# Kernel tuning notes

Measured on AMD Instinct MI355X. Metric: run time of the kernel, lower is better.

## Reference

```python
import jax, jax.numpy as jnp
import numpy as np

# NOBlock config: no_dims_in=(8,8), input_dim=output_dim=128, rank=8, level_diff=1
B, N, V = 4, 2048, 1
G1, G2, C = 8, 8, 128   # in_shape = (8, 8, 128); m = G1*G2 = 64 grid cells per token
M = G1 * G2
R = 8                    # Tucker ranks: [8, 8, 8] in and out (min(dim, rank))
LEVEL_DIFF = 1
GRP = 4 ** LEVEL_DIFF    # quadtree group size for hierarchical residual


def _xavier(key, shape):
    lim = float(np.sqrt(6.0 / (shape[0] + shape[1])))
    return jax.random.uniform(key, shape, jnp.float32, -lim, lim)


def setup_inputs() -> dict:
    key = jax.random.key(0)
    ks = jax.random.split(key, 10)
    x = jax.random.normal(ks[0], (B, N, V, M, C), jnp.float32)
    # core ~ N(0, scale^2), scale = sqrt(2/(fan_in+fan_out)), fan = prod(ranks) = 8^3
    scale = float(np.sqrt(2.0 / (R ** 3 + R ** 3)))
    core = jax.random.normal(ks[1], (R, R, R, R, R, R), jnp.float32) * scale
    out_f0 = _xavier(ks[2], (G1, R))
    out_f1 = _xavier(ks[3], (G2, R))
    out_f2 = _xavier(ks[4], (C, R))
    in_f0 = _xavier(ks[5], (G1, R))
    in_f1 = _xavier(ks[6], (G2, R))
    in_f2 = _xavier(ks[7], (C, R))
    mask = jax.random.bernoulli(ks[8], 0.25, (B, N, M))  # True = masked cell
    return {"x": x, "core": core, "out_f0": out_f0, "out_f1": out_f1,
            "out_f2": out_f2, "in_f0": in_f0, "in_f1": in_f1, "in_f2": in_f2,
            "mask": mask}


def reference(x, core, out_f0, out_f1, out_f2, in_f0, in_f1, in_f2, mask):
    b, n, v = x.shape[:3]
    # --- CrossTuckerLayer: 'bnvade,ABCDEF,oA,pB,qC,aD,dE,eF->bnvopq' ---
    xr = x.reshape(b, n, v, G1, G2, C)
    # project onto in-factor rank spaces
    z = jnp.einsum('bnvade,aD,dE,eF->bnvDEF', xr, in_f0, in_f1, in_f2, optimize=True)
    # core contraction (out-ranks ABC x in-ranks DEF)
    z = jnp.einsum('bnvDEF,ABCDEF->bnvABC', z, core)
    # expand to output dims
    h = jnp.einsum('bnvABC,oA,pB,qC->bnvopq', z, out_f0, out_f1, out_f2, optimize=True)
    h = h.reshape(b, n, v, M, C)
    # residual connection
    h = h + x
    # --- get_residual: hierarchical masked mixing, level_diff = 1 ---
    h4 = h.reshape(b, n * v, M, C)                     # v = 1
    hg = h4.reshape(b, -1, GRP, M, C)                  # [b, n/4, 4, m, c]
    w = (~mask).reshape(b, -1, GRP, M, 1).sum(axis=2, keepdims=True).astype(h.dtype)
    out = (hg / (w + 1e-10)).sum(axis=2)               # [b, n/4, m, c]
    out = out * (w.sum(axis=2) != 0).astype(h.dtype)
    return out
```

## Files before the change

kernel.cpp:

```cpp
#include <hip/hip_runtime.h>
#include <cstdint>
#include <cstddef>


__device__ __forceinline__ float dot4(const float4 a, const float4 b, float s) {
    return fmaf(a.w, b.w, fmaf(a.z, b.z, fmaf(a.y, b.y, fmaf(a.x, b.x, s))));
}

__global__ void transpose_core(const float* __restrict__ core,
                               float* __restrict__ coreT) {
    const int tid = blockIdx.x * 256 + threadIdx.x;
    const int r = tid & 511, k4 = tid >> 9;
    ((float4*)coreT)[(size_t)k4 * 512 + r] =
        ((const float4*)core)[(size_t)r * 128 + k4];
}

__launch_bounds__(256, 3)
__global__ void k1_inproj(const float* __restrict__ x,
                          const float* __restrict__ if0,
                          const float* __restrict__ if1,
                          const float* __restrict__ if2,
                          float* __restrict__ xsum_out,
                          float* __restrict__ zz_ws)
{
    __shared__ float xs[64 * 132];
    __shared__ float t1[512];
    __shared__ float s_if2T[8 * 132];
    __shared__ float s_if0[64], s_if1[64];
    float* t2 = xs;

    const int t = threadIdx.x;
    const int g = blockIdx.x;

    for (int i = t; i < 1024; i += 256) {
        const int e = i & 127, F = i >> 7;
        s_if2T[F * 132 + e] = if2[e * 8 + F];
    }
    if (t < 64) { s_if0[t] = if0[t]; s_if1[t] = if1[t]; }

    const float4* xg4 = (const float4*)(x + (size_t)g * 4 * 8192);
    float4 acc[8];
    #pragma unroll
    for (int i = 0; i < 8; ++i) acc[i] = xg4[t + 256 * i];
    #pragma unroll
    for (int j = 1; j < 4; ++j) {
        float4 v[8];
        #pragma unroll
        for (int i = 0; i < 8; ++i) v[i] = xg4[(size_t)j * 2048 + t + 256 * i];
        #pragma unroll
        for (int i = 0; i < 8; ++i) {
            acc[i].x += v[i].x; acc[i].y += v[i].y;
            acc[i].z += v[i].z; acc[i].w += v[i].w;
        }
    }
    float4* xo = (float4*)xsum_out + (size_t)g * 2048;
    #pragma unroll
    for (int i = 0; i < 8; ++i) xo[t + 256 * i] = acc[i];
    #pragma unroll
    for (int i = 0; i < 8; ++i) {
        const int f4i = t + 256 * i;
        *(float4*)&xs[(f4i >> 5) * 132 + (f4i & 31) * 4] = acc[i];
    }
    __syncthreads();

    #pragma unroll
    for (int h = 0; h < 2; ++h) {
        const int id = t + 256 * h;
        const int m = id >> 3, F = id & 7;
        const float4* xr = (const float4*)(xs + m * 132);
        const float4* wr = (const float4*)(s_if2T + F * 132);
        float s0 = 0.f, s1 = 0.f;
        #pragma unroll
        for (int e4 = 0; e4 < 32; e4 += 2) {
            s0 = dot4(xr[e4],     wr[e4],     s0);
            s1 = dot4(xr[e4 + 1], wr[e4 + 1], s1);
        }
        t1[id] = s0 + s1;
    }
    __syncthreads();

    #pragma unroll
    for (int h = 0; h < 2; ++h) {
        const int id = t + 256 * h;
        const int E = id >> 6, a = (id >> 3) & 7, F = id & 7;
        float s = 0.f;
        #pragma unroll
        for (int d0 = 0; d0 < 8; ++d0) {
            const int d = (d0 + a) & 7;
            s = fmaf(t1[a * 64 + d * 8 + F], s_if1[d * 8 + E], s);
        }
        t2[id] = s;
    }
    __syncthreads();

    #pragma unroll
    for (int h = 0; h < 2; ++h) {
        const int id = t + 256 * h;
        const int D = id >> 6, E = (id >> 3) & 7, F = id & 7;
        float s = 0.f;
        #pragma unroll
        for (int a0 = 0; a0 < 8; ++a0) {
            const int a = (a0 + E) & 7;
            s = fmaf(t2[E * 64 + a * 8 + F], s_if0[a * 8 + D], s);
        }
        zz_ws[(size_t)g * 512 + id] = s;
    }
}

__launch_bounds__(256, 2)
__global__ void k2_core_outproj(const float* __restrict__ coreT,
                                const float* __restrict__ zz_ws,
                                const float* __restrict__ of0,
                                const float* __restrict__ of1,
                                const float* __restrict__ of2,
                                const int* __restrict__ mask,
                                float* __restrict__ out)
{
    __shared__ float zz[2048];
    __shared__ float z2[2048];
    __shared__ float s_of0T[64], s_of1T[64];
    __shared__ float s_winv[256];
    float* t1 = zz;
    float* t2 = z2;

    const int t = threadIdx.x;
    const int blk = blockIdx.x;
    const size_t g0 = (size_t)blk * 4;

    {
        const float4* zw = (const float4*)(zz_ws + g0 * 512);
        ((float4*)zz)[t]       = zw[t];
        ((float4*)zz)[t + 256] = zw[t + 256];
    }
    if (t < 64) {
        s_of0T[t] = of0[(t & 7) * 8 + (t >> 3)];
        s_of1T[t] = of1[(t & 7) * 8 + (t >> 3)];
    }
    {
        const int g = t >> 6, m = t & 63;
        const int* mp = mask + (g0 + g) * 4 * 64 + m;
        int cnt = 0;
        #pragma unroll
        for (int j = 0; j < 4; ++j) cnt += (mp[j * 64] == 0) ? 1 : 0;
        s_winv[t] = cnt ? 1.0f / (float)cnt : 0.0f;
    }
    __syncthreads();

    {
        const float4* cT = (const float4*)coreT;
        const float4* z4 = (const float4*)zz;
        float c0a[4] = {0,0,0,0}, c1a[4] = {0,0,0,0};
        float c0b[4] = {0,0,0,0}, c1b[4] = {0,0,0,0};
        for (int k4 = 0; k4 < 128; k4 += 2) {
            const float4 ca0 = cT[(size_t)k4 * 512 + t];
            const float4 ca1 = cT[(size_t)k4 * 512 + t + 256];
            const float4 cb0 = cT[(size_t)(k4 + 1) * 512 + t];
            const float4 cb1 = cT[(size_t)(k4 + 1) * 512 + t + 256];
            #pragma unroll
            for (int g = 0; g < 4; ++g) {
                const float4 za = z4[g * 128 + k4];
                const float4 zb = z4[g * 128 + k4 + 1];
                c0a[g] = dot4(ca0, za, c0a[g]);
                c1a[g] = dot4(ca1, za, c1a[g]);
                c0b[g] = dot4(cb0, zb, c0b[g]);
                c1b[g] = dot4(cb1, zb, c1b[g]);
            }
        }
        #pragma unroll
        for (int g = 0; g < 4; ++g) {
            z2[g * 512 + t]       = c0a[g] + c0b[g];
            z2[g * 512 + t + 256] = c1a[g] + c1b[g];
        }
    }
    __syncthreads();

    #pragma unroll
    for (int h = 0; h < 8; ++h) {
        const int id2 = t + 256 * h;
        const int g = id2 >> 9, rem = id2 & 511;
        const int o = rem >> 6, Bq = (rem >> 3) & 7, Cr = rem & 7;
        float s = 0.f;
        #pragma unroll
        for (int A = 0; A < 8; ++A)
            s = fmaf(z2[g * 512 + A * 64 + Bq * 8 + Cr], s_of0T[A * 8 + o], s);
        t1[id2] = s;
    }
    __syncthreads();

    #pragma unroll
    for (int h = 0; h < 8; ++h) {
        const int id2 = t + 256 * h;
        const int g = id2 >> 9, rem = id2 & 511;
        const int p = rem >> 6, o = (rem >> 3) & 7, Cr = rem & 7;
        float s = 0.f;
        #pragma unroll
        for (int B0 = 0; B0 < 8; ++B0) {
            const int Bq = (B0 + o) & 7;
            s = fmaf(t1[g * 512 + o * 64 + Bq * 8 + Cr], s_of1T[Bq * 8 + p], s);
        }
        t2[id2] = s;
    }
    __syncthreads();

    float4 w[4][2];
    {
        const int cc = (4 * t) & 127;
        #pragma unroll
        for (int c = 0; c < 4; ++c) {
            w[c][0] = *(const float4*)(of2 + (cc + c) * 8);
            w[c][1] = *(const float4*)(of2 + (cc + c) * 8 + 4);
        }
    }
    float4* out4 = (float4*)out;
    #pragma unroll
    for (int g = 0; g < 4; ++g) {
        const size_t obase = (g0 + g) * 2048;
        float4 xv[8];
        #pragma unroll
        for (int i = 0; i < 8; ++i) xv[i] = out4[obase + t + 256 * i];
        #pragma unroll
        for (int i = 0; i < 8; ++i) {
            const int m = (t >> 5) + 8 * i;
            const int o = m >> 3, p = m & 7;
            const float wv = s_winv[g * 64 + m];
            const int base = g * 512 + p * 64 + o * 8;
            const float4 v0 = *(const float4*)(t2 + base);
            const float4 v1 = *(const float4*)(t2 + base + 4);
            float4 r;
            r.x = dot4(v1, w[0][1], dot4(v0, w[0][0], xv[i].x));
            r.y = dot4(v1, w[1][1], dot4(v0, w[1][0], xv[i].y));
            r.z = dot4(v1, w[2][1], dot4(v0, w[2][0], xv[i].z));
            r.w = dot4(v1, w[3][1], dot4(v0, w[3][0], xv[i].w));
            r.x *= wv; r.y *= wv; r.z *= wv; r.w *= wv;
            out4[obase + t + 256 * i] = r;
        }
    }
}

template<bool TR>
__launch_bounds__(256, 3)
__global__ void noblock_kernel(const float* __restrict__ x,
                               const float* __restrict__ core,
                               const float* __restrict__ coreT,
                               const float* __restrict__ of0,
                               const float* __restrict__ of1,
                               const float* __restrict__ of2,
                               const float* __restrict__ if0,
                               const float* __restrict__ if1,
                               const float* __restrict__ if2,
                               const int* __restrict__ mask,
                               float* __restrict__ out)
{
    __shared__ float xs[64 * 132];
    __shared__ float t1[512];
    __shared__ float t2[512];
    __shared__ float zz[2 * 512];
    __shared__ float z2[2 * 512];
    __shared__ float s_if2T[8 * 132];
    __shared__ float s_if0[64], s_if1[64];
    __shared__ float s_of0T[64], s_of1T[64];
    __shared__ float s_winv[128];

    const int t = threadIdx.x;
    const int blk = blockIdx.x;

    for (int i = t; i < 1024; i += 256) {
        const int e = i & 127, F = i >> 7;
        s_if2T[F * 132 + e] = if2[e * 8 + F];
    }
    if (t < 64) {
        s_if0[t] = if0[t];
        s_if1[t] = if1[t];
        s_of0T[t] = of0[(t & 7) * 8 + (t >> 3)];
        s_of1T[t] = of1[(t & 7) * 8 + (t >> 3)];
    }
    if (t < 128) {
        const int g = t >> 6, mm = t & 63;
        const int* mp = mask + ((size_t)(blk * 2 + g) * 4) * 64 + mm;
        int cnt = 0;
        #pragma unroll
        for (int j = 0; j < 4; ++j) cnt += (mp[j * 64] == 0) ? 1 : 0;
        s_winv[t] = cnt ? 1.0f / (float)cnt : 0.0f;
    }

    float4 acc[2][8];
    const float4* xg4 = (const float4*)(x + (size_t)blk * 8 * 8192);
    #pragma unroll
    for (int g = 0; g < 2; ++g)
        #pragma unroll
        for (int i = 0; i < 8; ++i)
            acc[g][i] = xg4[(size_t)(g * 4) * 2048 + t + 256 * i];
    #pragma unroll
    for (int j = 1; j < 4; ++j) {
        #pragma unroll
        for (int g = 0; g < 2; ++g) {
            float4 v[8];
            #pragma unroll
            for (int i = 0; i < 8; ++i)
                v[i] = xg4[(size_t)(g * 4 + j) * 2048 + t + 256 * i];
            #pragma unroll
            for (int i = 0; i < 8; ++i) {
                acc[g][i].x += v[i].x; acc[g][i].y += v[i].y;
                acc[g][i].z += v[i].z; acc[g][i].w += v[i].w;
            }
        }
    }

    #pragma unroll
    for (int g = 0; g < 2; ++g) {
        #pragma unroll
        for (int i = 0; i < 8; ++i) {
            const int f4i = t + 256 * i;
            *(float4*)&xs[(f4i >> 5) * 132 + (f4i & 31) * 4] = acc[g][i];
        }
        __syncthreads();
        #pragma unroll
        for (int h = 0; h < 2; ++h) {
            const int id = t + 256 * h;
            const int m = id >> 3, F = id & 7;
            const float4* xr = (const float4*)(xs + m * 132);
            const float4* wr = (const float4*)(s_if2T + F * 132);
            float s0 = 0.f, s1 = 0.f;
            #pragma unroll
            for (int e4 = 0; e4 < 32; e4 += 2) {
                s0 = dot4(xr[e4],     wr[e4],     s0);
                s1 = dot4(xr[e4 + 1], wr[e4 + 1], s1);
            }
            t1[id] = s0 + s1;
        }
        __syncthreads();
        #pragma unroll
        for (int h = 0; h < 2; ++h) {
            const int id = t + 256 * h;
            const int E = id >> 6, a = (id >> 3) & 7, F = id & 7;
            float s = 0.f;
            #pragma unroll
            for (int d0 = 0; d0 < 8; ++d0) {
                const int d = (d0 + a) & 7;
                s = fmaf(t1[a * 64 + d * 8 + F], s_if1[d * 8 + E], s);
            }
            t2[id] = s;
        }
        __syncthreads();
        #pragma unroll
        for (int h = 0; h < 2; ++h) {
            const int id = t + 256 * h;
            const int D = id >> 6, E = (id >> 3) & 7, F = id & 7;
            float s = 0.f;
            #pragma unroll
            for (int a0 = 0; a0 < 8; ++a0) {
                const int a = (a0 + E) & 7;
                s = fmaf(t2[E * 64 + a * 8 + F], s_if0[a * 8 + D], s);
            }
            zz[g * 512 + id] = s;
        }
        __syncthreads();
    }

    if (TR) {
        const float4* cT = (const float4*)coreT;
        const float4* z4 = (const float4*)zz;
        float a00 = 0.f, a01 = 0.f, a10 = 0.f, a11 = 0.f;
        float b00 = 0.f, b01 = 0.f, b10 = 0.f, b11 = 0.f;
        #pragma unroll 2
        for (int k4 = 0; k4 < 128; k4 += 2) {
            const float4 c0  = cT[(size_t)k4 * 512 + t];
            const float4 c1  = cT[(size_t)k4 * 512 + t + 256];
            const float4 c0b = cT[(size_t)(k4 + 1) * 512 + t];
            const float4 c1b = cT[(size_t)(k4 + 1) * 512 + t + 256];
            const float4 z0  = z4[k4],     z1  = z4[128 + k4];
            const float4 z0b = z4[k4 + 1], z1b = z4[128 + k4 + 1];
            a00 = dot4(c0,  z0,  a00);  a01 = dot4(c0,  z1,  a01);
            a10 = dot4(c1,  z0,  a10);  a11 = dot4(c1,  z1,  a11);
            b00 = dot4(c0b, z0b, b00);  b01 = dot4(c0b, z1b, b01);
            b10 = dot4(c1b, z0b, b10);  b11 = dot4(c1b, z1b, b11);
        }
        z2[t]             = a00 + b00;
        z2[t + 256]       = a10 + b10;
        z2[512 + t]       = a01 + b01;
        z2[512 + t + 256] = a11 + b11;
    } else {
        const float4* cr0 = (const float4*)(core + (size_t)t * 512);
        const float4* cr1 = (const float4*)(core + (size_t)(t + 256) * 512);
        const float4* z4 = (const float4*)zz;
        float a0[2] = {0.f, 0.f}, a1[2] = {0.f, 0.f};
        for (int kk = 0; kk < 128; ++kk) {
            const float4 c0 = cr0[kk], c1 = cr1[kk];
            #pragma unroll
            for (int g = 0; g < 2; ++g) {
                const float4 zv = z4[g * 128 + kk];
                a0[g] = dot4(c0, zv, a0[g]);
                a1[g] = dot4(c1, zv, a1[g]);
            }
        }
        #pragma unroll
        for (int g = 0; g < 2; ++g) {
            z2[g * 512 + t]       = a0[g];
            z2[g * 512 + t + 256] = a1[g];
        }
    }
    __syncthreads();

    float4 w[4][2];
    {
        const int cc = (4 * t) & 127;
        #pragma unroll
        for (int c = 0; c < 4; ++c) {
            w[c][0] = *(const float4*)(of2 + (cc + c) * 8);
            w[c][1] = *(const float4*)(of2 + (cc + c) * 8 + 4);
        }
    }

    float4* out4 = (float4*)out;
    #pragma unroll
    for (int g = 0; g < 2; ++g) {
        #pragma unroll
        for (int h = 0; h < 2; ++h) {
            const int id = t + 256 * h;
            const int o = id >> 6, Bq = (id >> 3) & 7, Cr = id & 7;
            float s = 0.f;
            #pragma unroll
            for (int A = 0; A < 8; ++A)
                s = fmaf(z2[g * 512 + A * 64 + Bq * 8 + Cr], s_of0T[A * 8 + o], s);
            t1[id] = s;
        }
        __syncthreads();
        #pragma unroll
        for (int h = 0; h < 2; ++h) {
            const int id = t + 256 * h;
            const int p = id >> 6, o = (id >> 3) & 7, Cr = id & 7;
            float s = 0.f;
            #pragma unroll
            for (int B0 = 0; B0 < 8; ++B0) {
                const int Bq = (B0 + o) & 7;
                s = fmaf(t1[o * 64 + Bq * 8 + Cr], s_of1T[Bq * 8 + p], s);
            }
            t2[id] = s;
        }
        __syncthreads();
        #pragma unroll
        for (int i = 0; i < 8; ++i) {
            const int m = (t >> 5) + 8 * i;
            const int o = m >> 3, p = m & 7;
            const float wv = s_winv[g * 64 + m];
            const int base = p * 64 + o * 8;
            const float4 v0 = *(const float4*)(t2 + base);
            const float4 v1 = *(const float4*)(t2 + base + 4);
            float4 r;
            r.x = dot4(v1, w[0][1], dot4(v0, w[0][0], acc[g][i].x));
            r.y = dot4(v1, w[1][1], dot4(v0, w[1][0], acc[g][i].y));
            r.z = dot4(v1, w[2][1], dot4(v0, w[2][0], acc[g][i].z));
            r.w = dot4(v1, w[3][1], dot4(v0, w[3][0], acc[g][i].w));
            r.x *= wv; r.y *= wv; r.z *= wv; r.w *= wv;
            out4[(size_t)(blk * 2 + g) * 2048 + t + 256 * i] = r;
        }
        __syncthreads();
    }
}

extern "C" void kernel_launch(void* const* d_in, const int* in_sizes, int n_in,
                              void* d_out, int out_size, void* d_ws, size_t ws_size,
                              hipStream_t stream) {
    const float* x    = (const float*)d_in[0];
    const float* core = (const float*)d_in[1];
    const float* of0  = (const float*)d_in[2];
    const float* of1  = (const float*)d_in[3];
    const float* of2  = (const float*)d_in[4];
    const float* if0  = (const float*)d_in[5];
    const float* if1  = (const float*)d_in[6];
    const float* if2  = (const float*)d_in[7];
    const int* mask   = (const int*)d_in[8];
    float* out = (float*)d_out;

    const size_t CORE_T_BYTES = (size_t)512 * 512 * 4;
    const size_t ZZ_BYTES     = (size_t)2048 * 512 * 4;

    if (d_ws && ws_size >= CORE_T_BYTES + ZZ_BYTES) {
        float* coreT = (float*)d_ws;
        float* zz_ws = (float*)((char*)d_ws + CORE_T_BYTES);
        transpose_core<<<dim3(256), dim3(256), 0, stream>>>(core, coreT);
        k1_inproj<<<dim3(2048), dim3(256), 0, stream>>>(
            x, if0, if1, if2, out, zz_ws);
        k2_core_outproj<<<dim3(512), dim3(256), 0, stream>>>(
            coreT, zz_ws, of0, of1, of2, mask, out);
    } else if (d_ws && ws_size >= CORE_T_BYTES) {
        float* coreT = (float*)d_ws;
        transpose_core<<<dim3(256), dim3(256), 0, stream>>>(core, coreT);
        noblock_kernel<true><<<dim3(1024), dim3(256), 0, stream>>>(
            x, core, coreT, of0, of1, of2, if0, if1, if2, mask, out);
    } else {
        noblock_kernel<false><<<dim3(1024), dim3(256), 0, stream>>>(
            x, core, core, of0, of1, of2, if0, if1, if2, mask, out);
    }
}
```

Before: 122.5 us.

## Fold core transpose into k1, shrink k1 LDS, widen k2 to 512 threads

Removes the separate transpose_core launch by having the first 64 blocks of k1_inproj do the core transpose, which saves one kernel launch. k1 reuses the xs buffer for t1 and t2, adding an extra barrier, so its LDS footprint drops and its occupancy hint rises from 3 to 4. k2 now runs 512 threads per block, each handling one core row instead of two, which halves per-thread registers and loop work. The unused template fallback path is also simplified. The trade-offs are extra barriers in k1 and fewer blocks per CU in k2.

Result: faster. 116.8 us (-4.7%).

```diff
diff --git a/kernel.cpp b/kernel.cpp
--- a/kernel.cpp
+++ b/kernel.cpp
@@ -7,16 +7,10 @@
     return fmaf(a.w, b.w, fmaf(a.z, b.z, fmaf(a.y, b.y, fmaf(a.x, b.x, s))));
 }
 
-__global__ void transpose_core(const float* __restrict__ core,
-                               float* __restrict__ coreT) {
-    const int tid = blockIdx.x * 256 + threadIdx.x;
-    const int r = tid & 511, k4 = tid >> 9;
-    ((float4*)coreT)[(size_t)k4 * 512 + r] =
-        ((const float4*)core)[(size_t)r * 128 + k4];
-}
-
-__launch_bounds__(256, 3)
+__launch_bounds__(256, 4)
 __global__ void k1_inproj(const float* __restrict__ x,
+                          const float* __restrict__ core,
+                          float* __restrict__ coreT,
                           const float* __restrict__ if0,
                           const float* __restrict__ if1,
                           const float* __restrict__ if2,
@@ -24,13 +18,27 @@
                           float* __restrict__ zz_ws)
 {
     __shared__ float xs[64 * 132];
-    __shared__ float t1[512];
     __shared__ float s_if2T[8 * 132];
     __shared__ float s_if0[64], s_if1[64];
-    float* t2 = xs;
+    float* t1 = xs;
+    float* t2 = xs + 512;
 
     const int t = threadIdx.x;
-    const int g = blockIdx.x;
+    const int blk = blockIdx.x;
+
+    if (blk < 64) {
+        const int tid = blk * 256 + t;
+        const float4* c4 = (const float4*)core;
+        float4* cT4 = (float4*)coreT;
+        #pragma unroll
+        for (int q = 0; q < 4; ++q) {
+            const int idx = tid + 16384 * q;
+            const int r = idx & 511, k4 = idx >> 9;
+            cT4[(size_t)k4 * 512 + r] = c4[(size_t)r * 128 + k4];
+        }
+        return;
+    }
+    const int g = blk - 64;
 
     for (int i = t; i < 1024; i += 256) {
         const int e = i & 127, F = i >> 7;
@@ -63,6 +71,7 @@
     }
     __syncthreads();
 
+    float r0, r1;
     #pragma unroll
     for (int h = 0; h < 2; ++h) {
         const int id = t + 256 * h;
@@ -75,8 +84,11 @@
             s0 = dot4(xr[e4],     wr[e4],     s0);
             s1 = dot4(xr[e4 + 1], wr[e4 + 1], s1);
         }
-        t1[id] = s0 + s1;
-    }
+        if (h == 0) r0 = s0 + s1; else r1 = s0 + s1;
+    }
+    __syncthreads();
+    t1[t] = r0;
+    t1[t + 256] = r1;
     __syncthreads();
 
     #pragma unroll
@@ -107,7 +119,7 @@
     }
 }
 
-__launch_bounds__(256, 2)
+__launch_bounds__(512, 2)
 __global__ void k2_core_outproj(const float* __restrict__ coreT,
                                 const float* __restrict__ zz_ws,
                                 const float* __restrict__ of0,
@@ -124,19 +136,14 @@
     float* t2 = z2;
 
     const int t = threadIdx.x;
-    const int blk = blockIdx.x;
-    const size_t g0 = (size_t)blk * 4;
-
-    {
-        const float4* zw = (const float4*)(zz_ws + g0 * 512);
-        ((float4*)zz)[t]       = zw[t];
-        ((float4*)zz)[t + 256] = zw[t + 256];
-    }
+    const size_t g0 = (size_t)blockIdx.x * 4;
+
+    ((float4*)zz)[t] = ((const float4*)(zz_ws + g0 * 512))[t];
     if (t < 64) {
         s_of0T[t] = of0[(t & 7) * 8 + (t >> 3)];
         s_of1T[t] = of1[(t & 7) * 8 + (t >> 3)];
     }
-    {
+    if (t < 256) {
         const int g = t >> 6, m = t & 63;
         const int* mp = mask + (g0 + g) * 4 * 64 + m;
         int cnt = 0;
@@ -149,34 +156,24 @@
     {
         const float4* cT = (const float4*)coreT;
         const float4* z4 = (const float4*)zz;
-        float c0a[4] = {0,0,0,0}, c1a[4] = {0,0,0,0};
-        float c0b[4] = {0,0,0,0}, c1b[4] = {0,0,0,0};
+        float a0[4] = {0, 0, 0, 0}, a1[4] = {0, 0, 0, 0};
         for (int k4 = 0; k4 < 128; k4 += 2) {
-            const float4 ca0 = cT[(size_t)k4 * 512 + t];
-            const float4 ca1 = cT[(size_t)k4 * 512 + t + 256];
-            const float4 cb0 = cT[(size_t)(k4 + 1) * 512 + t];
-            const float4 cb1 = cT[(size_t)(k4 + 1) * 512 + t + 256];
+            const float4 c0 = cT[(size_t)k4 * 512 + t];
+            const float4 c1 = cT[(size_t)(k4 + 1) * 512 + t];
             #pragma unroll
             for (int g = 0; g < 4; ++g) {
-                const float4 za = z4[g * 128 + k4];
-                const float4 zb = z4[g * 128 + k4 + 1];
-                c0a[g] = dot4(ca0, za, c0a[g]);
-                c1a[g] = dot4(ca1, za, c1a[g]);
-                c0b[g] = dot4(cb0, zb, c0b[g]);
-                c1b[g] = dot4(cb1, zb, c1b[g]);
-            }
-        }
-        #pragma unroll
-        for (int g = 0; g < 4; ++g) {
-            z2[g * 512 + t]       = c0a[g] + c0b[g];
-            z2[g * 512 + t + 256] = c1a[g] + c1b[g];
-        }
-    }
-    __syncthreads();
-
-    #pragma unroll
-    for (int h = 0; h < 8; ++h) {
-        const int id2 = t + 256 * h;
+                a0[g] = dot4(c0, z4[g * 128 + k4],     a0[g]);
+                a1[g] = dot4(c1, z4[g * 128 + k4 + 1], a1[g]);
+            }
+        }
+        #pragma unroll
+        for (int g = 0; g < 4; ++g) z2[g * 512 + t] = a0[g] + a1[g];
+    }
+    __syncthreads();
+
+    #pragma unroll
+    for (int h = 0; h < 4; ++h) {
+        const int id2 = t + 512 * h;
         const int g = id2 >> 9, rem = id2 & 511;
         const int o = rem >> 6, Bq = (rem >> 3) & 7, Cr = rem & 7;
         float s = 0.f;
@@ -188,8 +185,8 @@
     __syncthreads();
 
     #pragma unroll
-    for (int h = 0; h < 8; ++h) {
-        const int id2 = t + 256 * h;
+    for (int h = 0; h < 4; ++h) {
+        const int id2 = t + 512 * h;
         const int g = id2 >> 9, rem = id2 & 511;
         const int p = rem >> 6, o = (rem >> 3) & 7, Cr = rem & 7;
         float s = 0.f;
@@ -215,12 +212,12 @@
     #pragma unroll
     for (int g = 0; g < 4; ++g) {
         const size_t obase = (g0 + g) * 2048;
-        float4 xv[8];
-        #pragma unroll
-        for (int i = 0; i < 8; ++i) xv[i] = out4[obase + t + 256 * i];
-        #pragma unroll
-        for (int i = 0; i < 8; ++i) {
-            const int m = (t >> 5) + 8 * i;
+        float4 xv[4];
+        #pragma unroll
+        for (int i = 0; i < 4; ++i) xv[i] = out4[obase + t + 512 * i];
+        #pragma unroll
+        for (int i = 0; i < 4; ++i) {
+            const int m = (t >> 5) + 16 * i;
             const int o = m >> 3, p = m & 7;
             const float wv = s_winv[g * 64 + m];
             const int base = g * 512 + p * 64 + o * 8;
@@ -232,24 +229,22 @@
             r.z = dot4(v1, w[2][1], dot4(v0, w[2][0], xv[i].z));
             r.w = dot4(v1, w[3][1], dot4(v0, w[3][0], xv[i].w));
             r.x *= wv; r.y *= wv; r.z *= wv; r.w *= wv;
-            out4[obase + t + 256 * i] = r;
+            out4[obase + t + 512 * i] = r;
         }
     }
 }
 
-template<bool TR>
 __launch_bounds__(256, 3)
-__global__ void noblock_kernel(const float* __restrict__ x,
-                               const float* __restrict__ core,
-                               const float* __restrict__ coreT,
-                               const float* __restrict__ of0,
-                               const float* __restrict__ of1,
-                               const float* __restrict__ of2,
-                               const float* __restrict__ if0,
-                               const float* __restrict__ if1,
-                               const float* __restrict__ if2,
-                               const int* __restrict__ mask,
-                               float* __restrict__ out)
+__global__ void noblock_fused(const float* __restrict__ x,
+                              const float* __restrict__ core,
+                              const float* __restrict__ of0,
+                              const float* __restrict__ of1,
+                              const float* __restrict__ of2,
+                              const float* __restrict__ if0,
+                              const float* __restrict__ if1,
+                              const float* __restrict__ if2,
+                              const int* __restrict__ mask,
+                              float* __restrict__ out)
 {
     __shared__ float xs[64 * 132];
     __shared__ float t1[512];
@@ -357,29 +352,7 @@
         __syncthreads();
     }
 
-    if (TR) {
-        const float4* cT = (const float4*)coreT;
-        const float4* z4 = (const float4*)zz;
-        float a00 = 0.f, a01 = 0.f, a10 = 0.f, a11 = 0.f;
-        float b00 = 0.f, b01 = 0.f, b10 = 0.f, b11 = 0.f;
-        #pragma unroll 2
-        for (int k4 = 0; k4 < 128; k4 += 2) {
-            const float4 c0  = cT[(size_t)k4 * 512 + t];
-            const float4 c1  = cT[(size_t)k4 * 512 + t + 256];
-            const float4 c0b = cT[(size_t)(k4 + 1) * 512 + t];
-            const float4 c1b = cT[(size_t)(k4 + 1) * 512 + t + 256];
-            const float4 z0  = z4[k4],     z1  = z4[128 + k4];
-            const float4 z0b = z4[k4 + 1], z1b = z4[128 + k4 + 1];
-            a00 = dot4(c0,  z0,  a00);  a01 = dot4(c0,  z1,  a01);
-            a10 = dot4(c1,  z0,  a10);  a11 = dot4(c1,  z1,  a11);
-            b00 = dot4(c0b, z0b, b00);  b01 = dot4(c0b, z1b, b01);
-            b10 = dot4(c1b, z0b, b10);  b11 = dot4(c1b, z1b, b11);
-        }
-        z2[t]             = a00 + b00;
-        z2[t + 256]       = a10 + b10;
-        z2[512 + t]       = a01 + b01;
-        z2[512 + t + 256] = a11 + b11;
-    } else {
+    {
         const float4* cr0 = (const float4*)(core + (size_t)t * 512);
         const float4* cr1 = (const float4*)(core + (size_t)(t + 256) * 512);
         const float4* z4 = (const float4*)zz;
@@ -478,18 +451,12 @@
     if (d_ws && ws_size >= CORE_T_BYTES + ZZ_BYTES) {
         float* coreT = (float*)d_ws;
         float* zz_ws = (float*)((char*)d_ws + CORE_T_BYTES);
-        transpose_core<<<dim3(256), dim3(256), 0, stream>>>(core, coreT);
-        k1_inproj<<<dim3(2048), dim3(256), 0, stream>>>(
-            x, if0, if1, if2, out, zz_ws);
-        k2_core_outproj<<<dim3(512), dim3(256), 0, stream>>>(
+        k1_inproj<<<dim3(2112), dim3(256), 0, stream>>>(
+            x, core, coreT, if0, if1, if2, out, zz_ws);
+        k2_core_outproj<<<dim3(512), dim3(512), 0, stream>>>(
             coreT, zz_ws, of0, of1, of2, mask, out);
-    } else if (d_ws && ws_size >= CORE_T_BYTES) {
-        float* coreT = (float*)d_ws;
-        transpose_core<<<dim3(256), dim3(256), 0, stream>>>(core, coreT);
-        noblock_kernel<true><<<dim3(1024), dim3(256), 0, stream>>>(
-            x, core, coreT, of0, of1, of2, if0, if1, if2, mask, out);
     } else {
-        noblock_kernel<false><<<dim3(1024), dim3(256), 0, stream>>>(
-            x, core, core, of0, of1, of2, if0, if1, if2, mask, out);
+        noblock_fused<<<dim3(1024), dim3(256), 0, stream>>>(
+            x, core, of0, of1, of2, if0, if1, if2, mask, out);
     }
 }
```
